# Kernel tuning notes

Measured on AMD Instinct MI355X. Metric: run time of the kernel, lower is better.

## Reference

```python
import jax, jax.numpy as jnp
import numpy as np

EMBED_DIM = 1024
NUM_HEADS = 16
HEAD_DIM = EMBED_DIM // NUM_HEADS
SCALE = HEAD_DIM ** -0.5
EPS = 1e-5


def _layer_norm(x, w, b):
    mu = jnp.mean(x, axis=-1, keepdims=True)
    var = jnp.mean(jnp.square(x - mu), axis=-1, keepdims=True)
    return (x - mu) * jax.lax.rsqrt(var + EPS) * w + b


def setup_inputs() -> dict:
    key = jax.random.key(0)
    ks = jax.random.split(key, 8)
    B, L, Lp, C = 8, 4096, 256, EMBED_DIM
    gain = 0.05  # xavier_uniform gain
    lim = gain * np.sqrt(6.0 / (C + C))
    return {
        "prompt": jax.random.normal(ks[0], (B, Lp, C), jnp.float32),
        "x": jax.random.normal(ks[1], (B, L, C), jnp.float32),
        "ln_q_w": jnp.ones((C,), jnp.float32),
        "ln_q_b": jnp.zeros((C,), jnp.float32),
        "ln_k_w": jnp.ones((C,), jnp.float32),
        "ln_k_b": jnp.zeros((C,), jnp.float32),
        "Wq": jax.random.uniform(ks[2], (C, C), jnp.float32, -lim, lim),
        "bq": jnp.zeros((C,), jnp.float32),
        "Wk": jax.random.uniform(ks[3], (C, C), jnp.float32, -lim, lim),
        "bk": jnp.zeros((C,), jnp.float32),
        "Wo": jax.random.uniform(ks[4], (C, C), jnp.float32, -lim, lim),
        "bo": jnp.zeros((C,), jnp.float32),
        "alpha": jnp.asarray(0.5, jnp.float32),
    }


def reference(prompt, x, ln_q_w, ln_q_b, ln_k_w, ln_k_b, Wq, bq, Wk, bk, Wo, bo, alpha):
    B, L, C = x.shape
    Lp = prompt.shape[1]
    H, D = NUM_HEADS, HEAD_DIM

    q = _layer_norm(prompt, ln_q_w, ln_q_b)
    k = _layer_norm(x, ln_k_w, ln_k_b)

    # torch Linear: y = x @ W^T + b (W is [out, in])
    Q = (q @ Wq.T + bq).reshape(B, Lp, H, D).transpose(0, 2, 1, 3)  # [B,H,Lp,D]
    K = (k @ Wk.T + bk).reshape(B, L, H, D).transpose(0, 2, 1, 3)   # [B,H,L,D]
    V = x.reshape(B, L, H, D).transpose(0, 2, 1, 3)                  # [B,H,L,D]

    Q = jnp.clip(Q, -10.0, 10.0)
    K = jnp.clip(K, -10.0, 10.0)

    scores = jnp.einsum('bhqd,bhkd->bhqk', Q, K) * SCALE
    scores = scores - jax.lax.stop_gradient(jnp.max(scores, axis=-1, keepdims=True))
    attn = jax.nn.softmax(scores, axis=-1)

    attn_out = jnp.einsum('bhqk,bhkd->bhqd', attn, V)
    attn_out = attn_out.transpose(0, 2, 1, 3).reshape(B, Lp, C)
    attn_out = attn_out @ Wo.T + bo

    global_signal = jnp.mean(attn_out, axis=1, keepdims=True)  # [B,1,C]
    a = jax.nn.sigmoid(alpha) * 0.3
    return x + a * global_signal
```

## Files before the change

kernel.cpp:

```cpp
#include <hip/hip_runtime.h>

typedef __attribute__((ext_vector_type(8))) short  short8;
typedef __attribute__((ext_vector_type(4))) float  floatx4;
typedef __attribute__((ext_vector_type(2))) unsigned int uint2v;

#define NS 8

__device__ __forceinline__ unsigned short f2b(float f) {
  union { float f; unsigned u; } c; c.f = f;
  unsigned r = c.u + 0x7FFFu + ((c.u >> 16) & 1u);
  return (unsigned short)(r >> 16);
}

__device__ __forceinline__ float b2f(unsigned short u) {
  union { unsigned u; float f; } c; c.u = (unsigned)u << 16;
  return c.f;
}

__device__ __forceinline__ unsigned cvt_pk_bf16(float a, float b) {
  unsigned r;
  asm("v_cvt_pk_bf16_f32 %0, %1, %2" : "=v"(r) : "v"(a), "v"(b));
  return r;
}

__device__ __forceinline__ void async_copy16(const void* g, void* l) {
  __builtin_amdgcn_global_load_lds(
      (const __attribute__((address_space(1))) void*)g,
      (__attribute__((address_space(3))) void*)l, 16, 0, 0);
}

__global__ __launch_bounds__(256) void ln_bf16_kernel(
    const float* __restrict__ src, const float* __restrict__ w,
    const float* __restrict__ bias, unsigned short* __restrict__ dst) {
  const size_t row = blockIdx.x;
  const int t = threadIdx.x;
  const float4 v = *(const float4*)&src[row * 1024 + t * 4];
  float s = v.x + v.y + v.z + v.w;
  float q = v.x * v.x + v.y * v.y + v.z * v.z + v.w * v.w;
#pragma unroll
  for (int m = 32; m >= 1; m >>= 1) {
    s += __shfl_xor(s, m, 64);
    q += __shfl_xor(q, m, 64);
  }
  __shared__ float ss[4], sq[4];
  if ((t & 63) == 0) { ss[t >> 6] = s; sq[t >> 6] = q; }
  __syncthreads();
  s = ss[0] + ss[1] + ss[2] + ss[3];
  q = sq[0] + sq[1] + sq[2] + sq[3];
  const float mu = s * (1.f / 1024.f);
  const float var = q * (1.f / 1024.f) - mu * mu;
  const float rs = rsqrtf(var + 1e-5f);
  const float4 wv = *(const float4*)&w[t * 4];
  const float4 bv = *(const float4*)&bias[t * 4];
  ushort4 o;
  o.x = f2b((v.x - mu) * rs * wv.x + bv.x);
  o.y = f2b((v.y - mu) * rs * wv.y + bv.y);
  o.z = f2b((v.z - mu) * rs * wv.z + bv.z);
  o.w = f2b((v.w - mu) * rs * wv.w + bv.w);
  *(ushort4*)&dst[row * 1024 + t * 4] = o;
}

__global__ __launch_bounds__(256) void conv_bf16_kernel(
    const float* __restrict__ src, unsigned short* __restrict__ dst) {
  const size_t i = (size_t)blockIdx.x * 256 + threadIdx.x;
  const float4 v = ((const float4*)src)[i];
  ushort4 o;
  o.x = f2b(v.x); o.y = f2b(v.y); o.z = f2b(v.z); o.w = f2b(v.w);
  ((ushort4*)dst)[i] = o;
}

__global__ __launch_bounds__(256) void vtrans_kernel(
    const float* __restrict__ x, unsigned short* __restrict__ Vbf) {
  const int bh = blockIdx.x, kb = blockIdx.y;
  const int b = bh >> 4, h = bh & 15;
  const int t = threadIdx.x;
  __shared__ __align__(16) unsigned short tile[256][68];
  const int row16 = t >> 4, c4 = t & 15;
  const float* xp = x + ((size_t)(b * 4096 + kb * 256 + row16) * 1024) + h * 64 + c4 * 4;
#pragma unroll
  for (int pass = 0; pass < 16; ++pass) {
    const int k = pass * 16 + row16;
    float4 v = *(const float4*)&xp[(size_t)pass * 16 * 1024];
    ushort4 o;
    o.x = f2b(v.x); o.y = f2b(v.y); o.z = f2b(v.z); o.w = f2b(v.w);
    *(ushort4*)&tile[k][c4 * 4] = o;
  }
  __syncthreads();
  const int d = t >> 2, kc = t & 3;
  unsigned short* vp = Vbf + ((size_t)bh * 64 + d) * 4096 + kb * 256 + kc * 64;
#pragma unroll
  for (int j = 0; j < 8; ++j) {
    short8 o;
#pragma unroll
    for (int e = 0; e < 8; ++e) o[e] = (short)tile[kc * 64 + j * 8 + e][d];
    *(short8*)&vp[j * 8] = o;
  }
}

__global__ __launch_bounds__(256) void gemm_bt_kernel(
    const unsigned short* __restrict__ A, const unsigned short* __restrict__ W,
    const float* __restrict__ bias, unsigned short* __restrict__ out, int M) {
  __shared__ __align__(16) unsigned short smem[2][128 * 64];
  unsigned short* As = smem[0];
  unsigned short* Bs = smem[1];
  const int tid = threadIdx.x;
  const int wave = tid >> 6, lane = tid & 63;
  const int quad = lane >> 4, l16 = lane & 15;
  const int chunk = gridDim.x >> 3;
  const int work = (blockIdx.x & 7) * chunk + (blockIdx.x >> 3);
  const size_t m0 = (size_t)(work >> 3) * 128;
  const int n0 = (work & 7) * 128;
  const int wm = (wave >> 1) * 64, wn = (wave & 1) * 64;
  const int r8 = lane >> 3, cvv = lane & 7;
  const int csrc = cvv ^ r8;

  floatx4 acc[4][4];
#pragma unroll
  for (int i = 0; i < 4; i++)
#pragma unroll
    for (int j = 0; j < 4; j++) acc[i][j] = (floatx4){0.f, 0.f, 0.f, 0.f};

  const unsigned short* gA = A + (m0 + wave * 32 + r8) * 1024 + csrc * 8;
  const unsigned short* gB = W + ((size_t)(n0 + wave * 32 + r8)) * 1024 + csrc * 8;

  for (int k0 = 0; k0 < 1024; k0 += 64) {
    __syncthreads();
#pragma unroll
    for (int it = 0; it < 4; ++it) {
      async_copy16(gA + (size_t)it * 8 * 1024 + k0, &As[(wave * 4 + it) * 512]);
      async_copy16(gB + (size_t)it * 8 * 1024 + k0, &Bs[(wave * 4 + it) * 512]);
    }
    __syncthreads();
#pragma unroll
    for (int kh = 0; kh < 2; ++kh) {
      short8 af[4], bf[4];
#pragma unroll
      for (int mi = 0; mi < 4; mi++) {
        int row = wm + mi * 16 + l16;
        af[mi] = *(const short8*)&As[row * 64 + (((kh * 4 + quad) ^ (row & 7)) * 8)];
      }
#pragma unroll
      for (int ni = 0; ni < 4; ni++) {
        int row = wn + ni * 16 + l16;
        bf[ni] = *(const short8*)&Bs[row * 64 + (((kh * 4 + quad) ^ (row & 7)) * 8)];
      }
#pragma unroll
      for (int mi = 0; mi < 4; mi++)
#pragma unroll
        for (int ni = 0; ni < 4; ni++)
          acc[mi][ni] = __builtin_amdgcn_mfma_f32_16x16x32_bf16(af[mi], bf[ni], acc[mi][ni], 0, 0, 0);
    }
  }

  __syncthreads();
  unsigned short* Cs = smem[0];
#pragma unroll
  for (int ni = 0; ni < 4; ni++) {
    int n = n0 + wn + ni * 16 + l16;
    float bv = bias[n];
    int c = wn + ni * 16 + l16;
#pragma unroll
    for (int mi = 0; mi < 4; mi++)
#pragma unroll
      for (int p = 0; p < 4; p++) {
        int r = wm + mi * 16 + quad * 4 + p;
        float v = acc[mi][ni][p] + bv;
        v = fminf(10.f, fmaxf(-10.f, v));
        int cc = c >> 3;
        Cs[r * 128 + ((cc ^ (r & 7)) * 8) + (c & 7)] = f2b(v);
      }
  }
  __syncthreads();
#pragma unroll
  for (int i = 0; i < 8; ++i) {
    int r = (tid >> 4) + 16 * i;
    int cc = tid & 15;
    short8 v = *(const short8*)&Cs[r * 128 + ((cc ^ (r & 7)) * 8)];
    *(short8*)&out[(m0 + r) * 1024 + n0 + cc * 8] = v;
  }
}

__global__ __launch_bounds__(256) void attn_kernel(
    const unsigned short* __restrict__ Qp,
    const unsigned short* __restrict__ Kp,
    const unsigned short* __restrict__ Vbf,
    unsigned short* __restrict__ Onum,
    float* __restrict__ lpart) {
  const int bh = blockIdx.x, split = blockIdx.y;
  const int b = bh >> 4, h = bh & 15;
  const int tid = threadIdx.x, wave = tid >> 6, lane = tid & 63;
  const int quad = lane >> 4, l16 = lane & 15;
  const int r8 = lane >> 3, cvv = lane & 7, csrc = cvv ^ r8;

  __shared__ __align__(16) unsigned short smem[16384];
  unsigned short* Ks = smem;
  unsigned short* Vs = smem + 4096;
  unsigned short* Pw = smem + 8192;

  short8 qf[4][2];
#pragma unroll
  for (int mi = 0; mi < 4; mi++)
#pragma unroll
    for (int kh = 0; kh < 2; kh++)
      qf[mi][kh] = *(const short8*)&Qp[(size_t)(b * 256 + wave * 64 + mi * 16 + l16) * 1024 +
                                       h * 64 + kh * 32 + quad * 8];

  floatx4 oacc[4][4];
  floatx4 lacc[4];
#pragma unroll
  for (int i = 0; i < 4; i++) {
    lacc[i] = (floatx4){0.f, 0.f, 0.f, 0.f};
#pragma unroll
    for (int j = 0; j < 4; j++) oacc[i][j] = (floatx4){0.f, 0.f, 0.f, 0.f};
  }
  short8 ones;
#pragma unroll
  for (int j = 0; j < 8; j++) ones[j] = (short)0x3F80;

  const int kbase = split * (4096 / NS);
  const int rowbase = (wave & 1) * 32;
  const bool isK = (wave < 2);
  const unsigned short* gK = Kp + ((size_t)(b * 4096 + kbase + rowbase + r8)) * 1024 +
                             h * 64 + csrc * 8;
  const unsigned short* gV = Vbf + ((size_t)(bh * 64 + rowbase + r8)) * 4096 +
                             kbase + csrc * 8;

  const int T = 4096 / NS / 64;
  unsigned short* Pb = Pw + wave * 2048;

  uint4 stg[4];
  if (isK) {
#pragma unroll
    for (int it = 0; it < 4; ++it)
      stg[it] = *(const uint4*)&gK[((size_t)it * 8) * 1024];
  } else {
#pragma unroll
    for (int it = 0; it < 4; ++it)
      stg[it] = *(const uint4*)&gV[(size_t)it * 8 * 4096];
  }

  for (int t = 0; t < T; ++t) {
    __syncthreads();
    if (isK) {
#pragma unroll
      for (int it = 0; it < 4; ++it)
        *(uint4*)((char*)Ks + (rowbase + it * 8) * 128 + lane * 16) = stg[it];
    } else {
#pragma unroll
      for (int it = 0; it < 4; ++it)
        *(uint4*)((char*)Vs + (rowbase + it * 8) * 128 + lane * 16) = stg[it];
    }
    __syncthreads();
    if (t + 1 < T) {
      if (isK) {
#pragma unroll
        for (int it = 0; it < 4; ++it)
          stg[it] = *(const uint4*)&gK[((size_t)(t + 1) * 64 + it * 8) * 1024];
      } else {
#pragma unroll
        for (int it = 0; it < 4; ++it)
          stg[it] = *(const uint4*)&gV[(size_t)it * 8 * 4096 + (t + 1) * 64];
      }
    }

#pragma unroll
    for (int mh = 0; mh < 2; ++mh) {
#pragma unroll
      for (int ni = 0; ni < 4; ++ni) {
        const int krow = ni * 16 + l16;
        const short8 kf0 = *(const short8*)&Ks[krow * 64 + ((quad ^ (krow & 7)) * 8)];
        const short8 kf1 = *(const short8*)&Ks[krow * 64 + (((4 + quad) ^ (krow & 7)) * 8)];
#pragma unroll
        for (int m2 = 0; m2 < 2; ++m2) {
          const int mi = mh * 2 + m2;
          floatx4 st = (floatx4){0.f, 0.f, 0.f, 0.f};
          st = __builtin_amdgcn_mfma_f32_16x16x32_bf16(kf0, qf[mi][0], st, 0, 0, 0);
          st = __builtin_amdgcn_mfma_f32_16x16x32_bf16(kf1, qf[mi][1], st, 0, 0, 0);
          const float C = 0.18033688011112042f;
          float e0 = exp2f(st[0] * C);
          float e1 = exp2f(st[1] * C);
          float e2 = exp2f(st[2] * C);
          float e3 = exp2f(st[3] * C);
          unsigned lo = cvt_pk_bf16(e0, e1);
          unsigned hi = cvt_pk_bf16(e2, e3);
          const int qrow = m2 * 16 + l16;
          const int chunk = (ni * 2 + (quad >> 1)) ^ (qrow & 7);
          uint2v wv; wv.x = lo; wv.y = hi;
          *(uint2v*)&Pb[qrow * 64 + chunk * 8 + (quad & 1) * 4] = wv;
        }
      }
#pragma unroll
      for (int kh = 0; kh < 2; ++kh) {
        short8 vf[4];
#pragma unroll
        for (int ni = 0; ni < 4; ni++) {
          int row = ni * 16 + l16;
          vf[ni] = *(const short8*)&Vs[row * 64 + (((kh * 4 + quad) ^ (row & 7)) * 8)];
        }
#pragma unroll
        for (int m2 = 0; m2 < 2; ++m2) {
          const int mi = mh * 2 + m2;
          const int qrow = m2 * 16 + l16;
          short8 pf = *(const short8*)&Pb[qrow * 64 + (((kh * 4 + quad) ^ (qrow & 7)) * 8)];
#pragma unroll
          for (int ni = 0; ni < 4; ni++)
            oacc[mi][ni] = __builtin_amdgcn_mfma_f32_16x16x32_bf16(pf, vf[ni], oacc[mi][ni], 0, 0, 0);
          lacc[mi] = __builtin_amdgcn_mfma_f32_16x16x32_bf16(pf, ones, lacc[mi], 0, 0, 0);
        }
      }
    }
  }

  __syncthreads();
  unsigned short* Cs = smem;
#pragma unroll
  for (int mi = 0; mi < 4; mi++)
#pragma unroll
    for (int ni = 0; ni < 4; ni++)
#pragma unroll
      for (int p = 0; p < 4; p++) {
        int q = wave * 64 + mi * 16 + quad * 4 + p;
        int d = ni * 16 + l16;
        int cc = d >> 3;
        Cs[q * 64 + ((cc ^ (q & 7)) * 8) + (d & 7)] = f2b(oacc[mi][ni][p]);
      }
  __syncthreads();
  unsigned short* Ob = Onum + ((size_t)bh * NS + split) * 256 * 64;
#pragma unroll
  for (int i = 0; i < 8; ++i) {
    int q = (tid >> 3) + 32 * i;
    int cc = tid & 7;
    short8 v = *(const short8*)&Cs[q * 64 + ((cc ^ (q & 7)) * 8)];
    *(short8*)&Ob[q * 64 + cc * 8] = v;
  }
  if (l16 == 0) {
    float* lb = lpart + ((size_t)bh * NS + split) * 256;
#pragma unroll
    for (int mi = 0; mi < 4; mi++)
#pragma unroll
      for (int p = 0; p < 4; p++)
        lb[wave * 64 + mi * 16 + quad * 4 + p] = lacc[mi][p];
  }
}

__global__ __launch_bounds__(256) void reduce_heads_kernel(
    const unsigned short* __restrict__ Onum, const float* __restrict__ lpart,
    float* __restrict__ ho) {
  const int bh = blockIdx.x;
  const int t = threadIdx.x;
  __shared__ float ls[256];
  __shared__ float red[16][64];
  float l = 0.f;
#pragma unroll
  for (int s = 0; s < NS; s++) l += lpart[((size_t)bh * NS + s) * 256 + t];
  ls[t] = l;
  __syncthreads();
  const int d4 = t & 15, qg = t >> 4;
  float4 part = {0.f, 0.f, 0.f, 0.f};
  for (int qi = 0; qi < 16; ++qi) {
    int q = qg * 16 + qi;
    float4 on = {0.f, 0.f, 0.f, 0.f};
#pragma unroll
    for (int s = 0; s < NS; s++) {
      ushort4 v = *(const ushort4*)&Onum[(((size_t)bh * NS + s) * 256 + q) * 64 + d4 * 4];
      on.x += b2f(v.x); on.y += b2f(v.y); on.z += b2f(v.z); on.w += b2f(v.w);
    }
    const float rl = 1.f / ls[q];
    part.x += on.x * rl; part.y += on.y * rl;
    part.z += on.z * rl; part.w += on.w * rl;
  }
  *(float4*)&red[qg][d4 * 4] = part;
  __syncthreads();
  if (t < 64) {
    float v = 0.f;
#pragma unroll
    for (int r = 0; r < 16; ++r) v += red[r][t];
    v *= (1.f / 256.f);
    int b = bh >> 4, h = bh & 15;
    ho[b * 1024 + h * 64 + t] = v;
  }
}

__global__ __launch_bounds__(256) void wo_proj_kernel(
    const float* __restrict__ ho, const float* __restrict__ Wo,
    const float* __restrict__ bo, float* __restrict__ gs) {
  const int b = blockIdx.x >> 2, cg = blockIdx.x & 3;
  const int t = threadIdx.x;
  __shared__ float hs[1024];
#pragma unroll
  for (int i = 0; i < 4; i++) hs[t + i * 256] = ho[b * 1024 + t + i * 256];
  __syncthreads();
  const int c = cg * 256 + t;
  const float* wrow = Wo + (size_t)c * 1024;
  float acc = bo[c];
  for (int k = 0; k < 1024; k += 4) {
    float4 w4 = *(const float4*)&wrow[k];
    acc += w4.x * hs[k] + w4.y * hs[k + 1] + w4.z * hs[k + 2] + w4.w * hs[k + 3];
  }
  gs[b * 1024 + c] = acc;
}

__global__ __launch_bounds__(256) void final_add_kernel(
    const float* __restrict__ x, const float* __restrict__ gs,
    const float* __restrict__ alpha, float* __restrict__ out) {
  const float a = 0.3f / (1.f + __expf(-alpha[0]));
  const size_t i4 = (size_t)blockIdx.x * 256 + threadIdx.x;
  const float4 xv = ((const float4*)x)[i4];
  const float4 g = *(const float4*)&gs[(i4 >> 20) * 1024 + (i4 & 255) * 4];
  float4 o;
  o.x = xv.x + a * g.x; o.y = xv.y + a * g.y;
  o.z = xv.z + a * g.z; o.w = xv.w + a * g.w;
  ((float4*)out)[i4] = o;
}

extern "C" void kernel_launch(void* const* d_in, const int* in_sizes, int n_in,
                              void* d_out, int out_size, void* d_ws, size_t ws_size,
                              hipStream_t stream) {
  const float* prompt = (const float*)d_in[0];
  const float* x      = (const float*)d_in[1];
  const float* lnqw   = (const float*)d_in[2];
  const float* lnqb   = (const float*)d_in[3];
  const float* lnkw   = (const float*)d_in[4];
  const float* lnkb   = (const float*)d_in[5];
  const float* Wq     = (const float*)d_in[6];
  const float* bq     = (const float*)d_in[7];
  const float* Wk     = (const float*)d_in[8];
  const float* bk     = (const float*)d_in[9];
  const float* Wo     = (const float*)d_in[10];
  const float* bo     = (const float*)d_in[11];
  const float* alpha  = (const float*)d_in[12];
  float* out = (float*)d_out;

  char* ws = (char*)d_ws;
  unsigned short* kln = (unsigned short*)(ws + 0);
  unsigned short* Vbf = (unsigned short*)(ws + 0);
  unsigned short* qln = (unsigned short*)(ws + 67108864);
  unsigned short* Wqb = (unsigned short*)(ws + 71303168);
  unsigned short* Wkb = (unsigned short*)(ws + 73400320);
  unsigned short* Qp  = (unsigned short*)(ws + 75497472);
  float* lpart        = (float*)(ws + 79691776);
  float* ho           = (float*)(ws + 80740352);
  float* gs           = (float*)(ws + 80773120);

  char* ob = (char*)d_out;
  unsigned short* Kp   = (unsigned short*)(ob + 0);
  unsigned short* Onum = (unsigned short*)(ob + 67108864);

  ln_bf16_kernel<<<32768, 256, 0, stream>>>(x, lnkw, lnkb, kln);
  ln_bf16_kernel<<<2048, 256, 0, stream>>>(prompt, lnqw, lnqb, qln);
  conv_bf16_kernel<<<1024, 256, 0, stream>>>(Wq, Wqb);
  conv_bf16_kernel<<<1024, 256, 0, stream>>>(Wk, Wkb);
  gemm_bt_kernel<<<128, 256, 0, stream>>>(qln, Wqb, bq, Qp, 2048);
  gemm_bt_kernel<<<2048, 256, 0, stream>>>(kln, Wkb, bk, Kp, 32768);
  vtrans_kernel<<<dim3(128, 16), 256, 0, stream>>>(x, Vbf);
  attn_kernel<<<dim3(128, NS), 256, 0, stream>>>(Qp, Kp, Vbf, Onum, lpart);
  reduce_heads_kernel<<<128, 256, 0, stream>>>(Onum, lpart, ho);
  wo_proj_kernel<<<32, 256, 0, stream>>>(ho, Wo, bo, gs);
  final_add_kernel<<<32768, 256, 0, stream>>>(x, gs, alpha, out);
}
```

Before: 581.0 us.

## Keep P in registers via permlane swap, double-buffer K/V with async LDS loads

The attention inner loop no longer writes P through shared memory. Instead, K rows are permuted so each lane's exp values can be rearranged into the PV MFMA operand with permlane32_swap. The row-sum is now a scalar sum in registers with a final cross-lane shuffle, replacing the extra MFMA against a ones vector. K/V tiles move from register-staged copies to global_load_lds async copies into two LDS buffers, which removes one barrier per tile. The risks are a subtler data layout and the hardware-specific permlane builtin, and the sum is taken in fp32 before bf16 rounding, which slightly changes the numerics.

```diff
diff --git a/kernel.cpp b/kernel.cpp
--- a/kernel.cpp
+++ b/kernel.cpp
@@ -3,6 +3,7 @@
 typedef __attribute__((ext_vector_type(8))) short  short8;
 typedef __attribute__((ext_vector_type(4))) float  floatx4;
 typedef __attribute__((ext_vector_type(2))) unsigned int uint2v;
+typedef __attribute__((ext_vector_type(4))) unsigned int uintx4;
 
 #define NS 8
 
@@ -21,6 +22,10 @@
   unsigned r;
   asm("v_cvt_pk_bf16_f32 %0, %1, %2" : "=v"(r) : "v"(a), "v"(b));
   return r;
+}
+
+__device__ __forceinline__ uint2v permswap32(unsigned a, unsigned b) {
+  return __builtin_amdgcn_permlane32_swap(a, b, false, false);
 }
 
 __device__ __forceinline__ void async_copy16(const void* g, void* l) {
@@ -192,10 +197,7 @@
   const int quad = lane >> 4, l16 = lane & 15;
   const int r8 = lane >> 3, cvv = lane & 7, csrc = cvv ^ r8;
 
-  __shared__ __align__(16) unsigned short smem[16384];
-  unsigned short* Ks = smem;
-  unsigned short* Vs = smem + 4096;
-  unsigned short* Pw = smem + 8192;
+  __shared__ __align__(16) unsigned short smem[2][8192];
 
   short8 qf[4][2];
 #pragma unroll
@@ -206,113 +208,98 @@
                                        h * 64 + kh * 32 + quad * 8];
 
   floatx4 oacc[4][4];
-  floatx4 lacc[4];
-#pragma unroll
-  for (int i = 0; i < 4; i++) {
-    lacc[i] = (floatx4){0.f, 0.f, 0.f, 0.f};
+#pragma unroll
+  for (int i = 0; i < 4; i++)
 #pragma unroll
     for (int j = 0; j < 4; j++) oacc[i][j] = (floatx4){0.f, 0.f, 0.f, 0.f};
-  }
-  short8 ones;
-#pragma unroll
-  for (int j = 0; j < 8; j++) ones[j] = (short)0x3F80;
-
-  const int kbase = split * (4096 / NS);
+  float lsum[4] = {0.f, 0.f, 0.f, 0.f};
+
+  int koff[4], voff[4];
+#pragma unroll
+  for (int ni = 0; ni < 4; ++ni) {
+    const int krow = ((l16 >> 3) << 5) | ((ni >> 1) << 4) | (((l16 >> 2) & 1) << 3) |
+                     ((ni & 1) << 2) | (l16 & 3);
+    koff[ni] = krow * 64 + ((quad ^ (krow & 7)) * 8);
+    const int vrow = ni * 16 + l16;
+    voff[ni] = 4096 + vrow * 64 + ((quad ^ (vrow & 7)) * 8);
+  }
+
+  const int kbase = split * 512;
   const int rowbase = (wave & 1) * 32;
   const bool isK = (wave < 2);
-  const unsigned short* gK = Kp + ((size_t)(b * 4096 + kbase + rowbase + r8)) * 1024 +
-                             h * 64 + csrc * 8;
-  const unsigned short* gV = Vbf + ((size_t)(bh * 64 + rowbase + r8)) * 4096 +
-                             kbase + csrc * 8;
-
-  const int T = 4096 / NS / 64;
-  unsigned short* Pb = Pw + wave * 2048;
-
-  uint4 stg[4];
-  if (isK) {
-#pragma unroll
-    for (int it = 0; it < 4; ++it)
-      stg[it] = *(const uint4*)&gK[((size_t)it * 8) * 1024];
-  } else {
-#pragma unroll
-    for (int it = 0; it < 4; ++it)
-      stg[it] = *(const uint4*)&gV[(size_t)it * 8 * 4096];
-  }
-
-  for (int t = 0; t < T; ++t) {
-    __syncthreads();
-    if (isK) {
+  const unsigned short* gsrc =
+      isK ? Kp + ((size_t)(b * 4096 + kbase + rowbase + r8)) * 1024 + h * 64 + csrc * 8
+          : Vbf + ((size_t)(bh * 64 + rowbase + r8)) * 4096 + kbase + csrc * 8;
+  const size_t itstep = isK ? (size_t)8 * 1024 : (size_t)8 * 4096;
+  const size_t tstep  = isK ? (size_t)64 * 1024 : (size_t)64;
+  const int ldsbase = (isK ? 0 : 4096) + rowbase * 64;
+
+#pragma unroll
+  for (int it = 0; it < 4; ++it)
+    async_copy16(gsrc + it * itstep, &smem[0][ldsbase + it * 8 * 64]);
+  __syncthreads();
+
+  for (int t = 0; t < 8; ++t) {
+    if (t < 7) {
+      unsigned short* dB = smem[(t + 1) & 1];
 #pragma unroll
       for (int it = 0; it < 4; ++it)
-        *(uint4*)((char*)Ks + (rowbase + it * 8) * 128 + lane * 16) = stg[it];
-    } else {
-#pragma unroll
-      for (int it = 0; it < 4; ++it)
-        *(uint4*)((char*)Vs + (rowbase + it * 8) * 128 + lane * 16) = stg[it];
+        async_copy16(gsrc + (size_t)(t + 1) * tstep + it * itstep,
+                     &dB[ldsbase + it * 8 * 64]);
+    }
+    const unsigned short* Bf = smem[t & 1];
+
+#pragma unroll
+    for (int mh = 0; mh < 2; ++mh) {
+      unsigned pa0[2][4], pa1[2][4];
+#pragma unroll
+      for (int nl = 0; nl < 2; ++nl) {
+        const short8 ka0 = *(const short8*)&Bf[koff[nl]];
+        const short8 ka1 = *(const short8*)&Bf[koff[nl] ^ 32];
+        const short8 kb0 = *(const short8*)&Bf[koff[nl + 2]];
+        const short8 kb1 = *(const short8*)&Bf[koff[nl + 2] ^ 32];
+#pragma unroll
+        for (int m2 = 0; m2 < 2; ++m2) {
+          const int mi = mh * 2 + m2;
+          floatx4 sa = (floatx4){0.f, 0.f, 0.f, 0.f};
+          floatx4 sb = (floatx4){0.f, 0.f, 0.f, 0.f};
+          sa = __builtin_amdgcn_mfma_f32_16x16x32_bf16(ka0, qf[mi][0], sa, 0, 0, 0);
+          sa = __builtin_amdgcn_mfma_f32_16x16x32_bf16(ka1, qf[mi][1], sa, 0, 0, 0);
+          sb = __builtin_amdgcn_mfma_f32_16x16x32_bf16(kb0, qf[mi][0], sb, 0, 0, 0);
+          sb = __builtin_amdgcn_mfma_f32_16x16x32_bf16(kb1, qf[mi][1], sb, 0, 0, 0);
+          const float C = 0.18033688011112042f;
+          float e0 = exp2f(sa[0] * C), e1 = exp2f(sa[1] * C);
+          float e2 = exp2f(sa[2] * C), e3 = exp2f(sa[3] * C);
+          float f0 = exp2f(sb[0] * C), f1 = exp2f(sb[1] * C);
+          float f2 = exp2f(sb[2] * C), f3 = exp2f(sb[3] * C);
+          lsum[mi] += ((e0 + e1) + (e2 + e3)) + ((f0 + f1) + (f2 + f3));
+          unsigned wa0 = cvt_pk_bf16(e0, e1), wa1 = cvt_pk_bf16(e2, e3);
+          unsigned wb0 = cvt_pk_bf16(f0, f1), wb1 = cvt_pk_bf16(f2, f3);
+          uint2v r0 = permswap32(wa0, wb0);
+          uint2v r1 = permswap32(wa1, wb1);
+          pa0[m2][2 * nl + 0] = r0.x; pa1[m2][2 * nl + 0] = r0.y;
+          pa0[m2][2 * nl + 1] = r1.x; pa1[m2][2 * nl + 1] = r1.y;
+        }
+      }
+#pragma unroll
+      for (int kh = 0; kh < 2; ++kh)
+#pragma unroll
+        for (int ni = 0; ni < 4; ++ni) {
+          const short8 vf = *(const short8*)&Bf[kh ? (voff[ni] ^ 32) : voff[ni]];
+#pragma unroll
+          for (int m2 = 0; m2 < 2; ++m2) {
+            union { uintx4 u; short8 s; } cv;
+            cv.u = kh ? (uintx4){pa1[m2][0], pa1[m2][1], pa1[m2][2], pa1[m2][3]}
+                      : (uintx4){pa0[m2][0], pa0[m2][1], pa0[m2][2], pa0[m2][3]};
+            oacc[mh * 2 + m2][ni] =
+                __builtin_amdgcn_mfma_f32_16x16x32_bf16(cv.s, vf, oacc[mh * 2 + m2][ni], 0, 0, 0);
+          }
+        }
     }
     __syncthreads();
-    if (t + 1 < T) {
-      if (isK) {
-#pragma unroll
-        for (int it = 0; it < 4; ++it)
-          stg[it] = *(const uint4*)&gK[((size_t)(t + 1) * 64 + it * 8) * 1024];
-      } else {
-#pragma unroll
-        for (int it = 0; it < 4; ++it)
-          stg[it] = *(const uint4*)&gV[(size_t)it * 8 * 4096 + (t + 1) * 64];
-      }
-    }
-
-#pragma unroll
-    for (int mh = 0; mh < 2; ++mh) {
-#pragma unroll
-      for (int ni = 0; ni < 4; ++ni) {
-        const int krow = ni * 16 + l16;
-        const short8 kf0 = *(const short8*)&Ks[krow * 64 + ((quad ^ (krow & 7)) * 8)];
-        const short8 kf1 = *(const short8*)&Ks[krow * 64 + (((4 + quad) ^ (krow & 7)) * 8)];
-#pragma unroll
-        for (int m2 = 0; m2 < 2; ++m2) {
-          const int mi = mh * 2 + m2;
-          floatx4 st = (floatx4){0.f, 0.f, 0.f, 0.f};
-          st = __builtin_amdgcn_mfma_f32_16x16x32_bf16(kf0, qf[mi][0], st, 0, 0, 0);
-          st = __builtin_amdgcn_mfma_f32_16x16x32_bf16(kf1, qf[mi][1], st, 0, 0, 0);
-          const float C = 0.18033688011112042f;
-          float e0 = exp2f(st[0] * C);
-          float e1 = exp2f(st[1] * C);
-          float e2 = exp2f(st[2] * C);
-          float e3 = exp2f(st[3] * C);
-          unsigned lo = cvt_pk_bf16(e0, e1);
-          unsigned hi = cvt_pk_bf16(e2, e3);
-          const int qrow = m2 * 16 + l16;
-          const int chunk = (ni * 2 + (quad >> 1)) ^ (qrow & 7);
-          uint2v wv; wv.x = lo; wv.y = hi;
-          *(uint2v*)&Pb[qrow * 64 + chunk * 8 + (quad & 1) * 4] = wv;
-        }
-      }
-#pragma unroll
-      for (int kh = 0; kh < 2; ++kh) {
-        short8 vf[4];
-#pragma unroll
-        for (int ni = 0; ni < 4; ni++) {
-          int row = ni * 16 + l16;
-          vf[ni] = *(const short8*)&Vs[row * 64 + (((kh * 4 + quad) ^ (row & 7)) * 8)];
-        }
-#pragma unroll
-        for (int m2 = 0; m2 < 2; ++m2) {
-          const int mi = mh * 2 + m2;
-          const int qrow = m2 * 16 + l16;
-          short8 pf = *(const short8*)&Pb[qrow * 64 + (((kh * 4 + quad) ^ (qrow & 7)) * 8)];
-#pragma unroll
-          for (int ni = 0; ni < 4; ni++)
-            oacc[mi][ni] = __builtin_amdgcn_mfma_f32_16x16x32_bf16(pf, vf[ni], oacc[mi][ni], 0, 0, 0);
-          lacc[mi] = __builtin_amdgcn_mfma_f32_16x16x32_bf16(pf, ones, lacc[mi], 0, 0, 0);
-        }
-      }
-    }
-  }
-
-  __syncthreads();
-  unsigned short* Cs = smem;
+  }
+
+  unsigned short* Cs = &smem[0][0];
 #pragma unroll
   for (int mi = 0; mi < 4; mi++)
 #pragma unroll
@@ -333,13 +320,18 @@
     short8 v = *(const short8*)&Cs[q * 64 + ((cc ^ (q & 7)) * 8)];
     *(short8*)&Ob[q * 64 + cc * 8] = v;
   }
-  if (l16 == 0) {
+#pragma unroll
+  for (int mi = 0; mi < 4; ++mi) {
+    float v = lsum[mi];
+    v += __shfl_xor(v, 16, 64);
+    v += __shfl_xor(v, 32, 64);
+    lsum[mi] = v;
+  }
+  if (quad == 0) {
     float* lb = lpart + ((size_t)bh * NS + split) * 256;
 #pragma unroll
-    for (int mi = 0; mi < 4; mi++)
-#pragma unroll
-      for (int p = 0; p < 4; p++)
-        lb[wave * 64 + mi * 16 + quad * 4 + p] = lacc[mi][p];
+    for (int mi = 0; mi < 4; ++mi)
+      lb[wave * 64 + mi * 16 + l16] = lsum[mi];
   }
 }
 
```

Result: faster. 560.2 us (-3.6%).
